# Optimization experiments

Hardware: AMD Instinct MI355X
Metric: run time of the kernel (lower is better)

## Reference

```python
import jax, jax.numpy as jnp
import numpy as np
import math

D_MODEL = 512
MAX_LEN = 5000
N_DIM_DIVIDE = 2
PE_DIM = D_MODEL // N_DIM_DIVIDE


def make_pe():
    # sinusoidal PE buffer, shape [MAX_LEN, PE_DIM]
    position = np.arange(MAX_LEN, dtype=np.float32)[:, None]
    div_term = np.exp(np.arange(0, PE_DIM, 2, dtype=np.float32) * (-math.log(10000.0) / PE_DIM))
    pe = np.zeros((MAX_LEN, PE_DIM), dtype=np.float32)
    pe[:, 0::2] = np.sin(position * div_term)
    pe[:, 1::2] = np.cos(position * div_term)
    return jnp.asarray(pe)


def setup_inputs() -> dict:
    key = jax.random.key(0)
    k1, k2 = jax.random.split(key)
    B, S = 16, 4096
    x = jax.random.normal(k1, (B, S, D_MODEL), dtype=jnp.float32)
    # PAD = 1, NOT PAD = 0; per-sample length = count of zeros in the row
    mask = jax.random.randint(k2, (B, S), 0, 2, dtype=jnp.int32)
    pe = make_pe()
    return {"x": x, "mask": mask, "pe": pe}


def reference(x, mask, pe):
    B, S, D = x.shape
    # per-sample lengths: number of non-pad (== 0) entries
    lengths = jnp.sum(mask == 0, axis=1)  # [B]
    pos = jnp.arange(S)  # [S]
    # pe[:, :L].flip(dims=[1,2]) == pe[L-1-pos, ::-1] for pos < L
    rev_feat_pe = pe[:, ::-1]  # [MAX_LEN, PE_DIM], feature-dim reversed
    idx = jnp.clip(lengths[:, None] - 1 - pos[None, :], 0, None)  # [B, S]
    valid = pos[None, :] < lengths[:, None]  # [B, S]
    add_rev = jnp.where(valid[:, :, None], rev_feat_pe[idx], 0.0)  # [B, S, PE_DIM]
    add_rev = jnp.tile(add_rev, (1, 1, N_DIM_DIVIDE))  # [B, S, D]
    # forward also adds the plain (unflipped) PE over the full seq_len
    base = jnp.tile(pe[:S], (1, N_DIM_DIVIDE))  # [S, D]
    return x + add_rev + base[None, :, :]
```

## Files before the change

### kernel.cpp

```cpp
#include <hip/hip_runtime.h>


#define B_SZ   16
#define S_LEN  4096
#define D_MOD  512
#define PE_D   256

typedef float v4f __attribute__((ext_vector_type(4)));

__global__ __launch_bounds__(256) void lengths_kernel(
    const int* __restrict__ mask, int* __restrict__ lengths)
{
    const int b   = blockIdx.x;
    const int tid = threadIdx.x;
    const int4* m4 = reinterpret_cast<const int4*>(mask + (size_t)b * S_LEN);

    int cnt = 0;
    #pragma unroll
    for (int i = 0; i < (S_LEN / 4) / 256; ++i) {
        int4 v = m4[tid + i * 256];
        cnt += (v.x == 0) + (v.y == 0) + (v.z == 0) + (v.w == 0);
    }
    #pragma unroll
    for (int off = 32; off > 0; off >>= 1)
        cnt += __shfl_down(cnt, off, 64);

    __shared__ int wsum[4];
    const int lane = tid & 63;
    const int wave = tid >> 6;
    if (lane == 0) wsum[wave] = cnt;
    __syncthreads();
    if (tid == 0)
        lengths[b] = wsum[0] + wsum[1] + wsum[2] + wsum[3];
}

__global__ __launch_bounds__(256) void pe_add_kernel(
    const float* __restrict__ x, const float* __restrict__ pe,
    const int* __restrict__ lengths, float* __restrict__ out)
{
    const int tid  = threadIdx.x;
    const int lane = tid & 63;
    const int wave = tid >> 6;
    const long row = (long)blockIdx.x * 4 + wave;
    const int b    = (int)(row >> 12);
    const int s    = (int)(row & (S_LEN - 1));
    const int d    = lane << 2;

    const long off = row * D_MOD + d;
    const v4f xv0 = __builtin_nontemporal_load(
        reinterpret_cast<const v4f*>(x + off));
    const v4f xv1 = __builtin_nontemporal_load(
        reinterpret_cast<const v4f*>(x + off + PE_D));
    const v4f pv = *reinterpret_cast<const v4f*>(pe + (size_t)s * PE_D + d);

    v4f r = {0.f, 0.f, 0.f, 0.f};
    const int L = lengths[b];
    if (s < L) {
        const int idx = L - 1 - s;
        const v4f rv = *reinterpret_cast<const v4f*>(
            pe + (size_t)idx * PE_D + (252 - d));
        r = (v4f){rv.w, rv.z, rv.y, rv.x};
    }

    v4f o0 = (xv0 + r) + pv;
    v4f o1 = (xv1 + r) + pv;
    __builtin_nontemporal_store(o0, reinterpret_cast<v4f*>(out + off));
    __builtin_nontemporal_store(o1, reinterpret_cast<v4f*>(out + off + PE_D));
}

extern "C" void kernel_launch(void* const* d_in, const int* in_sizes, int n_in,
                              void* d_out, int out_size, void* d_ws, size_t ws_size,
                              hipStream_t stream)
{
    const float* x    = (const float*)d_in[0];
    const int*   mask = (const int*)d_in[1];
    const float* pe   = (const float*)d_in[2];
    float* out        = (float*)d_out;
    int*   lengths    = (int*)d_ws;

    lengths_kernel<<<B_SZ, 256, 0, stream>>>(mask, lengths);

    const int n_rows = B_SZ * S_LEN;
    pe_add_kernel<<<n_rows / 4, 256, 0, stream>>>(x, pe, lengths, out);
}
```

Before: 226.3 us.

## Fuse mask length reduction into PE add kernel with two rows per wave

Removes the separate lengths kernel and its launch by having every block recount its sample's non-pad tokens from the mask before doing the elementwise add. Each wave now processes two rows, so there are half as many blocks. This saves one launch and the dependency gap between kernels. In exchange, every block redundantly reads 16KB of mask (mostly served from cache) and waits on a block barrier before issuing its x loads.

```diff
diff --git a/kernel.cpp b/kernel.cpp
--- a/kernel.cpp
+++ b/kernel.cpp
@@ -8,64 +8,58 @@
 
 typedef float v4f __attribute__((ext_vector_type(4)));
 
-__global__ __launch_bounds__(256) void lengths_kernel(
-    const int* __restrict__ mask, int* __restrict__ lengths)
+__global__ __launch_bounds__(256) void pe_fused_kernel(
+    const float* __restrict__ x, const int* __restrict__ mask,
+    const float* __restrict__ pe, float* __restrict__ out)
 {
-    const int b   = blockIdx.x;
-    const int tid = threadIdx.x;
+    const int tid  = threadIdx.x;
+    const int lane = tid & 63;
+    const int wave = tid >> 6;
+    const int b    = blockIdx.x >> 9;
+
     const int4* m4 = reinterpret_cast<const int4*>(mask + (size_t)b * S_LEN);
-
     int cnt = 0;
     #pragma unroll
-    for (int i = 0; i < (S_LEN / 4) / 256; ++i) {
+    for (int i = 0; i < 4; ++i) {
         int4 v = m4[tid + i * 256];
         cnt += (v.x == 0) + (v.y == 0) + (v.z == 0) + (v.w == 0);
     }
     #pragma unroll
     for (int off = 32; off > 0; off >>= 1)
         cnt += __shfl_down(cnt, off, 64);
-
     __shared__ int wsum[4];
-    const int lane = tid & 63;
-    const int wave = tid >> 6;
     if (lane == 0) wsum[wave] = cnt;
     __syncthreads();
-    if (tid == 0)
-        lengths[b] = wsum[0] + wsum[1] + wsum[2] + wsum[3];
-}
+    const int L = wsum[0] + wsum[1] + wsum[2] + wsum[3];
 
-__global__ __launch_bounds__(256) void pe_add_kernel(
-    const float* __restrict__ x, const float* __restrict__ pe,
-    const int* __restrict__ lengths, float* __restrict__ out)
-{
-    const int tid  = threadIdx.x;
-    const int lane = tid & 63;
-    const int wave = tid >> 6;
-    const long row = (long)blockIdx.x * 4 + wave;
-    const int b    = (int)(row >> 12);
-    const int s    = (int)(row & (S_LEN - 1));
-    const int d    = lane << 2;
+    const long r0 = (long)blockIdx.x * 8 + wave * 2;
+    const int d   = lane << 2;
 
-    const long off = row * D_MOD + d;
-    const v4f xv0 = __builtin_nontemporal_load(
-        reinterpret_cast<const v4f*>(x + off));
-    const v4f xv1 = __builtin_nontemporal_load(
-        reinterpret_cast<const v4f*>(x + off + PE_D));
-    const v4f pv = *reinterpret_cast<const v4f*>(pe + (size_t)s * PE_D + d);
+    #pragma unroll
+    for (int k = 0; k < 2; ++k) {
+        const long row = r0 + k;
+        const int s    = (int)(row & (S_LEN - 1));
+        const long off = row * D_MOD + d;
 
-    v4f r = {0.f, 0.f, 0.f, 0.f};
-    const int L = lengths[b];
-    if (s < L) {
-        const int idx = L - 1 - s;
-        const v4f rv = *reinterpret_cast<const v4f*>(
-            pe + (size_t)idx * PE_D + (252 - d));
-        r = (v4f){rv.w, rv.z, rv.y, rv.x};
+        const v4f xv0 = __builtin_nontemporal_load(
+            reinterpret_cast<const v4f*>(x + off));
+        const v4f xv1 = __builtin_nontemporal_load(
+            reinterpret_cast<const v4f*>(x + off + PE_D));
+        const v4f pv = *reinterpret_cast<const v4f*>(pe + (size_t)s * PE_D + d);
+
+        v4f r = {0.f, 0.f, 0.f, 0.f};
+        if (s < L) {
+            const int idx = L - 1 - s;
+            const v4f rv = *reinterpret_cast<const v4f*>(
+                pe + (size_t)idx * PE_D + (252 - d));
+            r = (v4f){rv.w, rv.z, rv.y, rv.x};
+        }
+
+        v4f o0 = (xv0 + r) + pv;
+        v4f o1 = (xv1 + r) + pv;
+        __builtin_nontemporal_store(o0, reinterpret_cast<v4f*>(out + off));
+        __builtin_nontemporal_store(o1, reinterpret_cast<v4f*>(out + off + PE_D));
     }
-
-    v4f o0 = (xv0 + r) + pv;
-    v4f o1 = (xv1 + r) + pv;
-    __builtin_nontemporal_store(o0, reinterpret_cast<v4f*>(out + off));
-    __builtin_nontemporal_store(o1, reinterpret_cast<v4f*>(out + off + PE_D));
 }
 
 extern "C" void kernel_launch(void* const* d_in, const int* in_sizes, int n_in,
@@ -76,10 +70,7 @@
     const int*   mask = (const int*)d_in[1];
     const float* pe   = (const float*)d_in[2];
     float* out        = (float*)d_out;
-    int*   lengths    = (int*)d_ws;
 
-    lengths_kernel<<<B_SZ, 256, 0, stream>>>(mask, lengths);
-
-    const int n_rows = B_SZ * S_LEN;
-    pe_add_kernel<<<n_rows / 4, 256, 0, stream>>>(x, pe, lengths, out);
+    const int n_blocks = (B_SZ * S_LEN) / 8;
+    pe_fused_kernel<<<n_blocks, 256, 0, stream>>>(x, mask, pe, out);
 }
```

New measurement: 227.7 us. About the same (+0.6%).
